# Kernel tuning notes

Measured on AMD Instinct MI355X. Metric: run time of the kernel, lower is better.

## Reference

```python
import jax, jax.numpy as jnp
import numpy as np

D_MODEL = 512
NUM_HEADS = 8
HEAD_DIM = D_MODEL // NUM_HEADS
WINDOW = 64


def setup_inputs() -> dict:
    key = jax.random.key(0)
    ks = jax.random.split(key, 9)
    B, L = 4, 2048
    s = 1.0 / np.sqrt(D_MODEL)
    return {
        "x": jax.random.normal(ks[0], (B, L, D_MODEL), dtype=jnp.float32),
        "Wq": jax.random.normal(ks[1], (D_MODEL, D_MODEL), dtype=jnp.float32) * s,
        "bq": jnp.zeros((D_MODEL,), jnp.float32),
        "Wk": jax.random.normal(ks[2], (D_MODEL, D_MODEL), dtype=jnp.float32) * s,
        "bk": jnp.zeros((D_MODEL,), jnp.float32),
        "Wv": jax.random.normal(ks[3], (D_MODEL, D_MODEL), dtype=jnp.float32) * s,
        "bv": jnp.zeros((D_MODEL,), jnp.float32),
        "Wo": jax.random.normal(ks[4], (D_MODEL, D_MODEL), dtype=jnp.float32) * s,
        "bo": jnp.zeros((D_MODEL,), jnp.float32),
    }


def reference(x, Wq, bq, Wk, bk, Wv, bv, Wo, bo):
    B, L, _ = x.shape
    # projections -> [B, H, L, Dh]
    def proj(W, b):
        return (x @ W + b).reshape(B, L, NUM_HEADS, HEAD_DIM).transpose(0, 2, 1, 3)
    q, k, v = proj(Wq, bq), proj(Wk, bk), proj(Wv, bv)
    scores = jnp.einsum("bhqd,bhkd->bhqk", q, k) / np.sqrt(HEAD_DIM)
    idx = jnp.arange(L)
    dist = jnp.abs(idx[None, :] - idx[:, None])  # [L, L]
    mask = dist > WINDOW
    scores = jnp.where(mask[None, None], -jnp.inf, scores)
    attn = jax.nn.softmax(scores, axis=-1)  # dropout p inert in eval
    out = jnp.einsum("bhqk,bhkd->bhqd", attn, v)
    out = out.transpose(0, 2, 1, 3).reshape(B, L, D_MODEL)
    return out @ Wo + bo
```

## Files before the change

### kernel.cpp

```cpp
#include <hip/hip_runtime.h>
#include <cstdint>
#include <cstddef>

typedef _Float16 f16;
typedef f16 f16x8 __attribute__((ext_vector_type(8)));
typedef f16 f16x4 __attribute__((ext_vector_type(4)));
typedef float floatx4 __attribute__((ext_vector_type(4)));

#define GAS __attribute__((address_space(1)))
#define LAS __attribute__((address_space(3)))

static constexpr int LSEQ = 2048;
static constexpr int NH   = 8;
static constexpr int DH   = 64;
static constexpr int DM   = 512;
static constexpr int WIN  = 64;
static constexpr int MR   = 4 * LSEQ;

__global__ __launch_bounds__(256) void prep_kernel(
    const float* __restrict__ x, f16* __restrict__ xb,
    const float* __restrict__ Wq, const float* __restrict__ Wk,
    const float* __restrict__ Wv, const float* __restrict__ Wo,
    f16* __restrict__ wt) {
    __shared__ float tile[32][33];
    int bid = blockIdx.x;
    if (bid < 4096) {
        int i = bid * 256 + threadIdx.x;
        float4 v = ((const float4*)x)[i];
        f16x4 o = { (f16)v.x, (f16)v.y, (f16)v.z, (f16)v.w };
        ((f16x4*)xb)[i] = o;
    } else {
        int id = bid - 4096;
        int z  = id >> 8, t = id & 255;
        const float* W = z == 0 ? Wq : z == 1 ? Wk : z == 2 ? Wv : Wo;
        f16* out = wt + (size_t)z * DM * DM;
        int c0 = (t & 15) * 32, r0 = (t >> 4) * 32;
        int tx = threadIdx.x & 31, ty = threadIdx.x >> 5;
        #pragma unroll
        for (int i = 0; i < 32; i += 8)
            tile[ty + i][tx] = W[(size_t)(r0 + ty + i) * DM + c0 + tx];
        __syncthreads();
        #pragma unroll
        for (int i = 0; i < 32; i += 8)
            out[(size_t)(c0 + ty + i) * DM + r0 + tx] = (f16)tile[tx][ty + i];
    }
}

template <bool QKV>
__global__ __launch_bounds__(256, 2) void gemm_kernel(
    const f16* __restrict__ A, const f16* __restrict__ Bt_base,
    const float* __restrict__ b0, const float* __restrict__ b1,
    const float* __restrict__ b2,
    f16* __restrict__ out_q, f16* __restrict__ out_k, f16* __restrict__ out_vt,
    float* __restrict__ out_f) {
    const int chunk = gridDim.x >> 3;
    const int hw  = blockIdx.x;
    const int lin = (hw & 7) * chunk + (hw >> 3);
    const int n0  = (lin & 3) * 128;
    const int m0  = ((lin >> 2) & 63) * 128;
    const int z   = QKV ? (lin >> 8) : 0;

    const f16* __restrict__ Bt = Bt_base + (size_t)z * (DM * DM);
    const float* __restrict__ bias = QKV ? (z == 0 ? b0 : z == 1 ? b1 : b2) : b0;

    __shared__ f16 As[2][128 * 64];
    __shared__ f16 Bs[2][128 * 64];

    const int tid  = threadIdx.x;
    const int wid  = tid >> 6;
    const int lane = tid & 63;
    const int l15  = lane & 15;
    const int l4   = lane >> 4;
    const int wr   = wid >> 1, wc = wid & 1;

    floatx4 acc[4][4] = {};

    const int c_ = wid * 64 + lane;

    auto stage = [&](int buf, int k0) {
        #pragma unroll
        for (int i = 0; i < 4; ++i) {
            int c   = i * 256 + c_;
            int row = c >> 3, cw = c & 7;
            int cs  = cw ^ (row & 7);
            const f16* ga = A  + (size_t)(m0 + row) * DM + k0 + cs * 8;
            const f16* gb = Bt + (size_t)(n0 + row) * DM + k0 + cs * 8;
            f16* la = &As[buf][(i * 256 + wid * 64) * 8];
            f16* lb = &Bs[buf][(i * 256 + wid * 64) * 8];
            __builtin_amdgcn_global_load_lds((const GAS void*)ga, (LAS void*)la, 16, 0, 0);
            __builtin_amdgcn_global_load_lds((const GAS void*)gb, (LAS void*)lb, 16, 0, 0);
        }
    };
    auto compute = [&](int buf) {
        #pragma unroll
        for (int ks = 0; ks < 2; ++ks) {
            f16x8 af[4], bfr[4];
            #pragma unroll
            for (int m = 0; m < 4; ++m) {
                int row = wr * 64 + m * 16 + l15;
                int kc  = (ks * 4 + l4) ^ (row & 7);
                af[m] = *(const f16x8*)(&As[buf][row * 64 + kc * 8]);
            }
            #pragma unroll
            for (int n = 0; n < 4; ++n) {
                int row = wc * 64 + n * 16 + l15;
                int kc  = (ks * 4 + l4) ^ (row & 7);
                bfr[n] = *(const f16x8*)(&Bs[buf][row * 64 + kc * 8]);
            }
            #pragma unroll
            for (int m = 0; m < 4; ++m)
                #pragma unroll
                for (int n = 0; n < 4; ++n)
                    acc[m][n] = __builtin_amdgcn_mfma_f32_16x16x32_f16(af[m], bfr[n], acc[m][n], 0, 0, 0);
        }
    };

    stage(0, 0);
    stage(1, 64);
    #pragma unroll
    for (int t = 0; t < 8; ++t) {
        if (t < 7) asm volatile("s_waitcnt vmcnt(8)" ::: "memory");
        else       asm volatile("s_waitcnt vmcnt(0)" ::: "memory");
        __builtin_amdgcn_sched_barrier(0);
        __builtin_amdgcn_s_barrier();
        __builtin_amdgcn_sched_barrier(0);
        compute(t & 1);
        if (t < 6) {
            __builtin_amdgcn_s_barrier();
            __builtin_amdgcn_sched_barrier(0);
            stage(t & 1, (t + 2) * 64);
        }
    }

    #pragma unroll
    for (int n = 0; n < 4; ++n) {
        int gcol = n0 + wc * 64 + n * 16 + l15;
        float bias_v = bias[gcol];
        #pragma unroll
        for (int m = 0; m < 4; ++m) {
            int grow0 = m0 + wr * 64 + m * 16 + l4 * 4;
            #pragma unroll
            for (int r = 0; r < 4; ++r) {
                int grow = grow0 + r;
                float v = acc[m][n][r] + bias_v;
                if constexpr (QKV) {
                    int b = grow >> 11, lp = grow & (LSEQ - 1);
                    int h = gcol >> 6,  d  = gcol & (DH - 1);
                    int bh = b * NH + h;
                    if (z == 0)
                        out_q[((size_t)bh * LSEQ + lp) * DH + d] = (f16)(v * 0.125f);
                    else if (z == 1)
                        out_k[((size_t)bh * LSEQ + lp) * DH + d] = (f16)v;
                    else
                        out_vt[((size_t)bh * DH + d) * LSEQ + lp] = (f16)v;
                } else {
                    out_f[(size_t)grow * DM + gcol] = v;
                }
            }
        }
    }
}

__global__ __launch_bounds__(256) void attn_kernel(const f16* __restrict__ Qb,
                                                   const f16* __restrict__ Kb,
                                                   const f16* __restrict__ Vt,
                                                   f16* __restrict__ Ob) {
    const int hw  = blockIdx.x;
    const int lin = (hw & 7) * 128 + (hw >> 3);
    const int bh    = lin >> 5;
    const int q0blk = (lin & 31) * 64;
    const int wid    = threadIdx.x >> 6;
    const int lane   = threadIdx.x & 63;
    const int l15    = lane & 15, l4 = lane >> 4;
    const int qbase  = q0blk + wid * 16;
    const int kstart = q0blk - WIN;

    const f16* __restrict__ Q = Qb + (size_t)bh * LSEQ * DH;
    const f16* __restrict__ K = Kb + (size_t)bh * LSEQ * DH;
    const f16* __restrict__ V = Vt + (size_t)bh * DH * LSEQ;

    __shared__ f16 Pl[4][16][232];

    f16x8 qf[2];
    #pragma unroll
    for (int ks = 0; ks < 2; ++ks)
        qf[ks] = *(const f16x8*)(Q + (size_t)(qbase + l15) * DH + ks * 32 + l4 * 8);

    floatx4 sc[12] = {};
    #pragma unroll
    for (int nt = 0; nt < 12; ++nt) {
        int key = kstart + nt * 16 + l15;
        int kcl = key < 0 ? 0 : (key > LSEQ - 1 ? LSEQ - 1 : key);
        #pragma unroll
        for (int ks = 0; ks < 2; ++ks) {
            f16x8 kf = *(const f16x8*)(K + (size_t)kcl * DH + ks * 32 + l4 * 8);
            sc[nt] = __builtin_amdgcn_mfma_f32_16x16x32_f16(qf[ks], kf, sc[nt], 0, 0, 0);
        }
    }

    float mx[4] = {-1e30f, -1e30f, -1e30f, -1e30f};
    #pragma unroll
    for (int nt = 0; nt < 12; ++nt) {
        int key = kstart + nt * 16 + l15;
        #pragma unroll
        for (int r = 0; r < 4; ++r) {
            int q = qbase + l4 * 4 + r;
            int dist = key - q; dist = dist < 0 ? -dist : dist;
            bool valid = (key >= 0) && (key < LSEQ) && (dist <= WIN);
            float s = valid ? sc[nt][r] : -1e30f;
            sc[nt][r] = s;
            mx[r] = fmaxf(mx[r], s);
        }
    }
    #pragma unroll
    for (int r = 0; r < 4; ++r)
        #pragma unroll
        for (int m = 1; m < 16; m <<= 1)
            mx[r] = fmaxf(mx[r], __shfl_xor(mx[r], m, 64));
    float sm[4] = {0.f, 0.f, 0.f, 0.f};
    #pragma unroll
    for (int nt = 0; nt < 12; ++nt)
        #pragma unroll
        for (int r = 0; r < 4; ++r) {
            float p = __expf(sc[nt][r] - mx[r]);
            sc[nt][r] = p;
            sm[r] += p;
        }
    #pragma unroll
    for (int r = 0; r < 4; ++r) {
        #pragma unroll
        for (int m = 1; m < 16; m <<= 1)
            sm[r] += __shfl_xor(sm[r], m, 64);
        sm[r] = 1.f / sm[r];
    }

    #pragma unroll
    for (int nt = 0; nt < 12; ++nt)
        #pragma unroll
        for (int r = 0; r < 4; ++r)
            Pl[wid][l4 * 4 + r][nt * 16 + l15] = (f16)(sc[nt][r] * sm[r]);
    __syncthreads();

    floatx4 oc[4] = {};
    #pragma unroll
    for (int ks = 0; ks < 6; ++ks) {
        f16x8 pf = *(const f16x8*)(&Pl[wid][l15][ks * 32 + l4 * 8]);
        int kb0 = kstart + ks * 32 + l4 * 8;
        int kbc = (kb0 < 0 || kb0 > LSEQ - 8) ? 0 : kb0;
        #pragma unroll
        for (int dt = 0; dt < 4; ++dt) {
            f16x8 vf = *(const f16x8*)(V + (size_t)(dt * 16 + l15) * LSEQ + kbc);
            oc[dt] = __builtin_amdgcn_mfma_f32_16x16x32_f16(pf, vf, oc[dt], 0, 0, 0);
        }
    }

    int b = bh >> 3, h = bh & 7;
    #pragma unroll
    for (int dt = 0; dt < 4; ++dt) {
        int d = dt * 16 + l15;
        #pragma unroll
        for (int r = 0; r < 4; ++r) {
            int q = qbase + l4 * 4 + r;
            Ob[((size_t)b * LSEQ + q) * DM + h * DH + d] = (f16)oc[dt][r];
        }
    }
}

extern "C" void kernel_launch(void* const* d_in, const int* in_sizes, int n_in,
                              void* d_out, int out_size, void* d_ws, size_t ws_size,
                              hipStream_t stream) {
    const float* x  = (const float*)d_in[0];
    const float* Wq = (const float*)d_in[1];
    const float* bq = (const float*)d_in[2];
    const float* Wk = (const float*)d_in[3];
    const float* bk = (const float*)d_in[4];
    const float* Wv = (const float*)d_in[5];
    const float* bv = (const float*)d_in[6];
    const float* Wo = (const float*)d_in[7];
    const float* bo = (const float*)d_in[8];
    float* out = (float*)d_out;

    char* ws = (char*)d_ws;
    f16* xb = (f16*)(ws);
    f16* wt = (f16*)(ws + (8ull << 20));
    f16* qb = (f16*)(ws + (10ull << 20));
    f16* kb = (f16*)(ws + (18ull << 20));
    f16* vt = (f16*)(ws + (26ull << 20));
    f16* ob = (f16*)(ws + (34ull << 20));

    prep_kernel<<<dim3(5120), 256, 0, stream>>>(x, xb, Wq, Wk, Wv, Wo, wt);
    gemm_kernel<true><<<dim3(768), 256, 0, stream>>>(
        xb, wt, bq, bk, bv, qb, kb, vt, nullptr);
    attn_kernel<<<dim3(1024), 256, 0, stream>>>(qb, kb, vt, ob);
    gemm_kernel<false><<<dim3(256), 256, 0, stream>>>(
        ob, wt + 3ull * DM * DM, bo, bo, bo, nullptr, nullptr, nullptr, out);
}
```

Measured before the change: 86.62 us.

## Stage full-K weight tile in LDS and stream activations directly from global

The GEMM tile changes from 128x128 to 256x64. The whole 64x512 weight slab is loaded once into LDS, and each wave reads its A fragments straight from global memory into registers, which removes the double-buffered A/B LDS pipeline and its barriers. The aim is to cut LDS staging and synchronisation overhead. In exchange, A loads go uncached through LDS with no explicit prefetch, LDS use rises to 64KB, which may lower occupancy, and the launch_bounds occupancy hint is dropped.

```diff
diff --git a/kernel.cpp b/kernel.cpp
--- a/kernel.cpp
+++ b/kernel.cpp
@@ -47,7 +47,7 @@
 }
 
 template <bool QKV>
-__global__ __launch_bounds__(256, 2) void gemm_kernel(
+__global__ __launch_bounds__(256) void gemm_kernel(
     const f16* __restrict__ A, const f16* __restrict__ Bt_base,
     const float* __restrict__ b0, const float* __restrict__ b1,
     const float* __restrict__ b2,
@@ -56,89 +56,61 @@
     const int chunk = gridDim.x >> 3;
     const int hw  = blockIdx.x;
     const int lin = (hw & 7) * chunk + (hw >> 3);
-    const int n0  = (lin & 3) * 128;
-    const int m0  = ((lin >> 2) & 63) * 128;
+    const int n0  = (lin & 7) * 64;
+    const int m0  = ((lin >> 3) & 31) * 256;
     const int z   = QKV ? (lin >> 8) : 0;
 
     const f16* __restrict__ Bt = Bt_base + (size_t)z * (DM * DM);
     const float* __restrict__ bias = QKV ? (z == 0 ? b0 : z == 1 ? b1 : b2) : b0;
 
-    __shared__ f16 As[2][128 * 64];
-    __shared__ f16 Bs[2][128 * 64];
+    __shared__ f16 Bs[64 * 512];
 
     const int tid  = threadIdx.x;
     const int wid  = tid >> 6;
     const int lane = tid & 63;
     const int l15  = lane & 15;
     const int l4   = lane >> 4;
-    const int wr   = wid >> 1, wc = wid & 1;
+    const int rbase = m0 + wid * 64;
+
+    #pragma unroll
+    for (int i = 0; i < 16; ++i) {
+        int gg  = i * 256 + tid;
+        int col = gg >> 6, gp = gg & 63;
+        int sg  = gp ^ (col & 7);
+        const f16* g = Bt + (size_t)(n0 + col) * DM + sg * 8;
+        f16* l = &Bs[(i * 256 + wid * 64) * 8];
+        __builtin_amdgcn_global_load_lds((const GAS void*)g, (LAS void*)l, 16, 0, 0);
+    }
+    __syncthreads();
 
     floatx4 acc[4][4] = {};
 
-    const int c_ = wid * 64 + lane;
-
-    auto stage = [&](int buf, int k0) {
-        #pragma unroll
-        for (int i = 0; i < 4; ++i) {
-            int c   = i * 256 + c_;
-            int row = c >> 3, cw = c & 7;
-            int cs  = cw ^ (row & 7);
-            const f16* ga = A  + (size_t)(m0 + row) * DM + k0 + cs * 8;
-            const f16* gb = Bt + (size_t)(n0 + row) * DM + k0 + cs * 8;
-            f16* la = &As[buf][(i * 256 + wid * 64) * 8];
-            f16* lb = &Bs[buf][(i * 256 + wid * 64) * 8];
-            __builtin_amdgcn_global_load_lds((const GAS void*)ga, (LAS void*)la, 16, 0, 0);
-            __builtin_amdgcn_global_load_lds((const GAS void*)gb, (LAS void*)lb, 16, 0, 0);
-        }
-    };
-    auto compute = [&](int buf) {
-        #pragma unroll
-        for (int ks = 0; ks < 2; ++ks) {
-            f16x8 af[4], bfr[4];
+    #pragma unroll 4
+    for (int ks = 0; ks < 16; ++ks) {
+        f16x8 af[4], bfr[4];
+        #pragma unroll
+        for (int m = 0; m < 4; ++m)
+            af[m] = *(const f16x8*)(A + (size_t)(rbase + m * 16 + l15) * DM + ks * 32 + l4 * 8);
+        #pragma unroll
+        for (int n = 0; n < 4; ++n) {
+            int col = n * 16 + l15;
+            int gp  = (ks * 4 + l4) ^ (col & 7);
+            bfr[n] = *(const f16x8*)(&Bs[col * 512 + gp * 8]);
+        }
+        #pragma unroll
+        for (int m = 0; m < 4; ++m)
             #pragma unroll
-            for (int m = 0; m < 4; ++m) {
-                int row = wr * 64 + m * 16 + l15;
-                int kc  = (ks * 4 + l4) ^ (row & 7);
-                af[m] = *(const f16x8*)(&As[buf][row * 64 + kc * 8]);
-            }
-            #pragma unroll
-            for (int n = 0; n < 4; ++n) {
-                int row = wc * 64 + n * 16 + l15;
-                int kc  = (ks * 4 + l4) ^ (row & 7);
-                bfr[n] = *(const f16x8*)(&Bs[buf][row * 64 + kc * 8]);
-            }
-            #pragma unroll
-            for (int m = 0; m < 4; ++m)
-                #pragma unroll
-                for (int n = 0; n < 4; ++n)
-                    acc[m][n] = __builtin_amdgcn_mfma_f32_16x16x32_f16(af[m], bfr[n], acc[m][n], 0, 0, 0);
-        }
-    };
-
-    stage(0, 0);
-    stage(1, 64);
-    #pragma unroll
-    for (int t = 0; t < 8; ++t) {
-        if (t < 7) asm volatile("s_waitcnt vmcnt(8)" ::: "memory");
-        else       asm volatile("s_waitcnt vmcnt(0)" ::: "memory");
-        __builtin_amdgcn_sched_barrier(0);
-        __builtin_amdgcn_s_barrier();
-        __builtin_amdgcn_sched_barrier(0);
-        compute(t & 1);
-        if (t < 6) {
-            __builtin_amdgcn_s_barrier();
-            __builtin_amdgcn_sched_barrier(0);
-            stage(t & 1, (t + 2) * 64);
-        }
+            for (int n = 0; n < 4; ++n)
+                acc[m][n] = __builtin_amdgcn_mfma_f32_16x16x32_f16(af[m], bfr[n], acc[m][n], 0, 0, 0);
     }
 
     #pragma unroll
     for (int n = 0; n < 4; ++n) {
-        int gcol = n0 + wc * 64 + n * 16 + l15;
+        int gcol = n0 + n * 16 + l15;
         float bias_v = bias[gcol];
         #pragma unroll
         for (int m = 0; m < 4; ++m) {
-            int grow0 = m0 + wr * 64 + m * 16 + l4 * 4;
+            int grow0 = rbase + m * 16 + l4 * 4;
             #pragma unroll
             for (int r = 0; r < 4; ++r) {
                 int grow = grow0 + r;
```

Measured after the change: 101.6 us. +17.3%, slower.

## Use 256x256-tile 8-wave QKV GEMM with interleaved staging and MFMA priority

Applied to the files above, without the earlier changes.

Replaces the templated 128x128 QKV projection GEMM with a dedicated kernel that uses 512 threads and 256x256 output tiles, so each block reuses its A and B tiles across more output. Global-to-LDS loads for the next K step are spread across the four sub-phases of the compute loop, and wave priority is raised around the MFMA bursts. The grid shrinks from 768 to 192 blocks, which is fewer than the number of CUs on the device and risks leaving some idle. The output projection is split into its own plain kernel with no functional change.

```diff
diff --git a/kernel.cpp b/kernel.cpp
--- a/kernel.cpp
+++ b/kernel.cpp
@@ -46,22 +46,148 @@
     }
 }
 
-template <bool QKV>
-__global__ __launch_bounds__(256, 2) void gemm_kernel(
+__global__ __launch_bounds__(512, 1) void gemm_qkv8(
     const f16* __restrict__ A, const f16* __restrict__ Bt_base,
     const float* __restrict__ b0, const float* __restrict__ b1,
     const float* __restrict__ b2,
-    f16* __restrict__ out_q, f16* __restrict__ out_k, f16* __restrict__ out_vt,
-    float* __restrict__ out_f) {
+    f16* __restrict__ out_q, f16* __restrict__ out_k, f16* __restrict__ out_vt) {
+    const int hw  = blockIdx.x;
+    const int lin = (hw & 7) * 24 + (hw >> 3);
+    const int z   = lin / 64;
+    const int rem = lin % 64;
+    const int m0  = (rem >> 1) * 256;
+    const int n0  = (rem & 1) * 256;
+
+    const f16* __restrict__ Bt = Bt_base + (size_t)z * DM * DM;
+    const float* __restrict__ bias = z == 0 ? b0 : z == 1 ? b1 : b2;
+
+    __shared__ f16 As[2][2][128 * 64];
+    __shared__ f16 Bs[2][2][128 * 64];
+
+    const int tid  = threadIdx.x;
+    const int wid  = tid >> 6;
+    const int lane = tid & 63;
+    const int l15  = lane & 15;
+    const int l4   = lane >> 4;
+    const int wrow = wid >> 2;
+    const int wcol = wid & 3;
+    const int bh_  = wcol >> 1;
+    const int bcl_ = (wcol & 1) * 64;
+
+    floatx4 acc[8][4] = {};
+
+    auto stageA = [&](int db, int h, int k0) {
+        #pragma unroll
+        for (int r = 0; r < 2; ++r) {
+            int c   = r * 512 + tid;
+            int row = c >> 3, cw = c & 7;
+            int cs  = cw ^ (row & 7);
+            const f16* g = A + (size_t)(m0 + h * 128 + row) * DM + k0 + cs * 8;
+            f16* l = &As[db][h][(r * 512 + wid * 64) * 8];
+            __builtin_amdgcn_global_load_lds((const GAS void*)g, (LAS void*)l, 16, 0, 0);
+        }
+    };
+    auto stageB = [&](int db, int h, int k0) {
+        #pragma unroll
+        for (int r = 0; r < 2; ++r) {
+            int c   = r * 512 + tid;
+            int row = c >> 3, cw = c & 7;
+            int cs  = cw ^ (row & 7);
+            const f16* g = Bt + (size_t)(n0 + h * 128 + row) * DM + k0 + cs * 8;
+            f16* l = &Bs[db][h][(r * 512 + wid * 64) * 8];
+            __builtin_amdgcn_global_load_lds((const GAS void*)g, (LAS void*)l, 16, 0, 0);
+        }
+    };
+
+    stageA(0, 0, 0); stageA(0, 1, 0); stageB(0, 0, 0); stageB(0, 1, 0);
+    asm volatile("s_waitcnt vmcnt(0)" ::: "memory");
+    __builtin_amdgcn_sched_barrier(0);
+    __builtin_amdgcn_s_barrier();
+
+    f16x8 bf[4][2];
+    #pragma unroll
+    for (int t = 0; t < 8; ++t) {
+        const int db  = t & 1;
+        const int k0n = (t + 1) * 64;
+        #pragma unroll
+        for (int p = 0; p < 4; ++p) {
+            if (p == 0) {
+                #pragma unroll
+                for (int n = 0; n < 4; ++n)
+                    #pragma unroll
+                    for (int kk = 0; kk < 2; ++kk) {
+                        int cl = bcl_ + n * 16 + l15;
+                        int kc = (kk * 4 + l4) ^ (cl & 7);
+                        bf[n][kk] = *(const f16x8*)(&Bs[db][bh_][cl * 64 + kc * 8]);
+                    }
+            }
+            f16x8 af[2][2];
+            #pragma unroll
+            for (int mi = 0; mi < 2; ++mi)
+                #pragma unroll
+                for (int kk = 0; kk < 2; ++kk) {
+                    int rl = (p * 2 + mi) * 16 + l15;
+                    int kc = (kk * 4 + l4) ^ (rl & 7);
+                    af[mi][kk] = *(const f16x8*)(&As[db][wrow][rl * 64 + kc * 8]);
+                }
+            if (t < 7) {
+                if (p == 0)      { stageA(db ^ 1, 0, k0n); stageA(db ^ 1, 1, k0n); }
+                else if (p == 1) { stageB(db ^ 1, 0, k0n); stageB(db ^ 1, 1, k0n); }
+            }
+            __builtin_amdgcn_s_barrier();
+            asm volatile("s_waitcnt lgkmcnt(0)" ::: "memory");
+            __builtin_amdgcn_sched_barrier(0);
+            __builtin_amdgcn_s_setprio(1);
+            #pragma unroll
+            for (int mi = 0; mi < 2; ++mi)
+                #pragma unroll
+                for (int n = 0; n < 4; ++n)
+                    #pragma unroll
+                    for (int kk = 0; kk < 2; ++kk)
+                        acc[p * 2 + mi][n] = __builtin_amdgcn_mfma_f32_16x16x32_f16(
+                            af[mi][kk], bf[n][kk], acc[p * 2 + mi][n], 0, 0, 0);
+            __builtin_amdgcn_s_setprio(0);
+            if (p == 3) {
+                asm volatile("s_waitcnt vmcnt(0)" ::: "memory");
+                __builtin_amdgcn_sched_barrier(0);
+            }
+            __builtin_amdgcn_s_barrier();
+        }
+    }
+
+    #pragma unroll
+    for (int n = 0; n < 4; ++n) {
+        int gcol = n0 + wcol * 64 + n * 16 + l15;
+        float bias_v = bias[gcol];
+        #pragma unroll
+        for (int m = 0; m < 8; ++m) {
+            int grow0 = m0 + wrow * 128 + m * 16 + l4 * 4;
+            #pragma unroll
+            for (int r = 0; r < 4; ++r) {
+                int grow = grow0 + r;
+                float v = acc[m][n][r] + bias_v;
+                int b = grow >> 11, lp = grow & (LSEQ - 1);
+                int h = gcol >> 6,  d  = gcol & (DH - 1);
+                int bh = b * NH + h;
+                if (z == 0)
+                    out_q[((size_t)bh * LSEQ + lp) * DH + d] = (f16)(v * 0.125f);
+                else if (z == 1)
+                    out_k[((size_t)bh * LSEQ + lp) * DH + d] = (f16)v;
+                else
+                    out_vt[((size_t)bh * DH + d) * LSEQ + lp] = (f16)v;
+            }
+        }
+    }
+}
+
+__global__ __launch_bounds__(256, 2) void gemm_out(
+    const f16* __restrict__ A, const f16* __restrict__ Bt,
+    const float* __restrict__ bo, float* __restrict__ out_f) {
     const int chunk = gridDim.x >> 3;
     const int hw  = blockIdx.x;
     const int lin = (hw & 7) * chunk + (hw >> 3);
     const int n0  = (lin & 3) * 128;
     const int m0  = ((lin >> 2) & 63) * 128;
-    const int z   = QKV ? (lin >> 8) : 0;
-
-    const f16* __restrict__ Bt = Bt_base + (size_t)z * (DM * DM);
-    const float* __restrict__ bias = QKV ? (z == 0 ? b0 : z == 1 ? b1 : b2) : b0;
 
     __shared__ f16 As[2][128 * 64];
     __shared__ f16 Bs[2][128 * 64];
@@ -74,7 +200,6 @@
     const int wr   = wid >> 1, wc = wid & 1;
 
     floatx4 acc[4][4] = {};
-
     const int c_ = wid * 64 + lane;
 
     auto stage = [&](int buf, int k0) {
@@ -135,28 +260,13 @@
     #pragma unroll
     for (int n = 0; n < 4; ++n) {
         int gcol = n0 + wc * 64 + n * 16 + l15;
-        float bias_v = bias[gcol];
+        float bias_v = bo[gcol];
         #pragma unroll
         for (int m = 0; m < 4; ++m) {
             int grow0 = m0 + wr * 64 + m * 16 + l4 * 4;
             #pragma unroll
-            for (int r = 0; r < 4; ++r) {
-                int grow = grow0 + r;
-                float v = acc[m][n][r] + bias_v;
-                if constexpr (QKV) {
-                    int b = grow >> 11, lp = grow & (LSEQ - 1);
-                    int h = gcol >> 6,  d  = gcol & (DH - 1);
-                    int bh = b * NH + h;
-                    if (z == 0)
-                        out_q[((size_t)bh * LSEQ + lp) * DH + d] = (f16)(v * 0.125f);
-                    else if (z == 1)
-                        out_k[((size_t)bh * LSEQ + lp) * DH + d] = (f16)v;
-                    else
-                        out_vt[((size_t)bh * DH + d) * LSEQ + lp] = (f16)v;
-                } else {
-                    out_f[(size_t)grow * DM + gcol] = v;
-                }
-            }
+            for (int r = 0; r < 4; ++r)
+                out_f[(size_t)(grow0 + r) * DM + gcol] = acc[m][n][r] + bias_v;
         }
     }
 }
@@ -289,9 +399,7 @@
     f16* ob = (f16*)(ws + (34ull << 20));
 
     prep_kernel<<<dim3(5120), 256, 0, stream>>>(x, xb, Wq, Wk, Wv, Wo, wt);
-    gemm_kernel<true><<<dim3(768), 256, 0, stream>>>(
-        xb, wt, bq, bk, bv, qb, kb, vt, nullptr);
+    gemm_qkv8<<<dim3(192), 512, 0, stream>>>(xb, wt, bq, bk, bv, qb, kb, vt);
     attn_kernel<<<dim3(1024), 256, 0, stream>>>(qb, kb, vt, ob);
-    gemm_kernel<false><<<dim3(256), 256, 0, stream>>>(
-        ob, wt + 3ull * DM * DM, bo, bo, bo, nullptr, nullptr, nullptr, out);
+    gemm_out<<<dim3(256), 256, 0, stream>>>(ob, wt + 3ull * DM * DM, bo, out);
 }
```

Result: slower. 93.51 us (+8.0%).
